# Kernel optimization log

Measured on AMD Instinct MI355X. Metric: run time of the kernel, lower is better.

Reference implementation:

```python
import jax, jax.numpy as jnp
import numpy as np

T = 4096
D = 512
H = 8
HD = D // H
DFF = D  # dim_ff = dmodel per module code
NUM_ACTIONS = 14
NUM_OBJECTS = 123
NEG = -1e9


def _layernorm(x, g, b, eps=1e-5):
    m = jnp.mean(x, axis=-1, keepdims=True)
    v = jnp.var(x, axis=-1, keepdims=True)
    return (x - m) / jnp.sqrt(v + eps) * g + b


def setup_inputs() -> dict:
    key = jax.random.key(0)
    ks = jax.random.split(key, 12)
    w = lambda k, s: (jax.random.normal(k, s) * 0.02).astype(jnp.float32)
    return {
        "action_seq": jax.random.randint(ks[0], (T, 2), 0, NUM_ACTIONS),
        "batch_id": jnp.sort(jax.random.randint(ks[1], (T,), 0, 16)),
        "W_type": w(ks[2], (NUM_ACTIONS, D)), "b_type": jnp.zeros((D,), jnp.float32),
        "W_arg": w(ks[3], (NUM_OBJECTS + 1, D)), "b_arg": jnp.zeros((D,), jnp.float32),
        "sos": jnp.zeros((D,), jnp.float32),
        "Wq": w(ks[4], (2, D, D)), "bq": jnp.zeros((2, D), jnp.float32),
        "Wk": w(ks[5], (2, D, D)), "bk": jnp.zeros((2, D), jnp.float32),
        "Wv": w(ks[6], (2, D, D)), "bv": jnp.zeros((2, D), jnp.float32),
        "Wo": w(ks[7], (2, D, D)), "bo": jnp.zeros((2, D), jnp.float32),
        "ln1_g": jnp.ones((2, D), jnp.float32), "ln1_b": jnp.zeros((2, D), jnp.float32),
        "W1": w(ks[8], (2, D, DFF)), "b1": jnp.zeros((2, DFF), jnp.float32),
        "W2": w(ks[9], (2, DFF, D)), "b2": jnp.zeros((2, D), jnp.float32),
        "ln2_g": jnp.ones((2, D), jnp.float32), "ln2_b": jnp.zeros((2, D), jnp.float32),
    }


def _forward(action_seq, batch_id, W_type, b_type, W_arg, b_arg, sos,
             Wq, bq, Wk, bk, Wv, bv, Wo, bo, ln1_g, ln1_b, W1, b1, W2, b2, ln2_g, ln2_b):
    Tn = action_seq.shape[0]
    dt = W_type.dtype
    # embeddings (one-hot @ W == Linear on one-hot)
    type_emb = jax.nn.one_hot(action_seq[:, 0], NUM_ACTIONS, dtype=dt) @ W_type + b_type
    arg_emb = jax.nn.one_hot(action_seq[:, 1] + 1, NUM_OBJECTS + 1, dtype=dt) @ W_arg + b_arg
    # position within each packed sequence (batch_id sorted-contiguous)
    seg_start = jnp.searchsorted(batch_id, batch_id, side='left')
    pos = (jnp.arange(Tn) - seg_start).astype(dt)
    div = jnp.exp(-jnp.log(10000.0) * jnp.arange(0, D, 2).astype(dt) / D)
    ang = pos[:, None] * div[None, :]
    pe = jnp.stack([jnp.sin(ang), jnp.cos(ang)], axis=-1).reshape(Tn, D)  # interleaved sin/cos
    x = jnp.concatenate([sos[None, :], type_emb + arg_emb + pe], axis=0)  # [T+1, D]
    T1 = Tn + 1
    # block-diagonal causal mask with prepended SOS token (always attendable)
    idx = jnp.arange(T1)
    bid1 = jnp.concatenate([jnp.full((1,), -1, dtype=batch_id.dtype), batch_id])
    allowed = (idx[:, None] >= idx[None, :]) & (bid1[:, None] == bid1[None, :])
    allowed = allowed | (idx[None, :] == 0)
    bias = jnp.where(allowed, 0.0, NEG).astype(dt)  # [T1, T1]
    scale = 1.0 / jnp.sqrt(jnp.asarray(HD, dtype=dt))
    for l in range(2):  # transformer_layer_a, transformer_layer_b
        q = (x @ Wq[l] + bq[l]).reshape(T1, H, HD)
        k = (x @ Wk[l] + bk[l]).reshape(T1, H, HD)
        v = (x @ Wv[l] + bv[l]).reshape(T1, H, HD)
        s = jnp.einsum('qhd,khd->hqk', q, k) * scale + bias[None, :, :]
        a = jax.nn.softmax(s, axis=-1)
        o = jnp.einsum('hqk,khd->qhd', a, v).reshape(T1, D) @ Wo[l] + bo[l]
        x = _layernorm(x + o, ln1_g[l], ln1_b[l])
        f = jax.nn.relu(x @ W1[l] + b1[l]) @ W2[l] + b2[l]
        x = _layernorm(x + f, ln2_g[l], ln2_b[l])
    return x  # [T+1, D]


def reference(action_seq, batch_id, W_type, b_type, W_arg, b_arg, sos,
              Wq, bq, Wk, bk, Wv, bv, Wo, bo, ln1_g, ln1_b, W1, b1, W2, b2, ln2_g, ln2_b):
    return _forward(action_seq, batch_id, W_type, b_type, W_arg, b_arg, sos,
                    Wq, bq, Wk, bk, Wv, bv, Wo, bo, ln1_g, ln1_b, W1, b1, W2, b2, ln2_g, ln2_b)
```

## Files before the change

kernel.cpp:

```cpp
#include <hip/hip_runtime.h>
#include <hip/hip_bf16.h>
#include <stdint.h>

#define T_TOK 4096
#define T1N   4097
#define DMODEL 512
#define VTS   4160

typedef __attribute__((ext_vector_type(8))) short bf16x8;
typedef __attribute__((ext_vector_type(4))) float f32x4;

static __device__ __forceinline__ unsigned short f2bf(float f) {
  __hip_bfloat16 h = __float2bfloat16(f);
  return *reinterpret_cast<unsigned short*>(&h);
}

__global__ __launch_bounds__(256) void wt_kernel(
    const float* __restrict__ Wq, const float* __restrict__ Wk,
    const float* __restrict__ Wv, const float* __restrict__ Wo,
    const float* __restrict__ W1, const float* __restrict__ W2,
    __hip_bfloat16* __restrict__ out) {
  int m = blockIdx.z;
  int kind = m >> 1, layer = m & 1;
  const float* src = kind==0?Wq: kind==1?Wk: kind==2?Wv: kind==3?Wo: kind==4?W1:W2;
  src += (size_t)layer*DMODEL*DMODEL;
  __hip_bfloat16* dst = out + (size_t)m*DMODEL*DMODEL;
  __shared__ float tile[32][33];
  int bn = blockIdx.x*32;
  int bk = blockIdx.y*32;
  int tx = threadIdx.x & 31, ty = threadIdx.x >> 5;
  for (int r = ty; r < 32; r += 8)
    tile[r][tx] = src[(size_t)(bk + r)*DMODEL + bn + tx];
  __syncthreads();
  for (int r = ty; r < 32; r += 8)
    dst[(size_t)(bn + r)*DMODEL + bk + tx] = __float2bfloat16(tile[tx][r]);
}

__global__ __launch_bounds__(256) void embed_kernel(
    const int* __restrict__ aseq, const int* __restrict__ bid,
    const float* __restrict__ Wt, const float* __restrict__ bt,
    const float* __restrict__ Wa, const float* __restrict__ ba,
    const float* __restrict__ sosv,
    float* __restrict__ x, __hip_bfloat16* __restrict__ xb,
    int* __restrict__ ss) {
  int i = blockIdx.x;
  int tid = threadIdx.x;
  int d0 = tid * 2;
  float o0, o1;
  if (i == 0) {
    o0 = sosv[d0]; o1 = sosv[d0+1];
  } else {
    int t = i - 1;
    int a0 = aseq[2*t], a1 = aseq[2*t+1];
    int key = bid[t];
    int lo = 0, hi = t;
    while (lo < hi) { int mid = (lo+hi) >> 1; if (bid[mid] < key) lo = mid + 1; else hi = mid; }
    if (tid == 0) ss[t] = lo;
    float pos = (float)(t - lo);
    float dv = __expf(-9.210340371976184f * (float)d0 * (1.0f/(float)DMODEL));
    float ang = pos * dv;
    float sn = sinf(ang), cs = cosf(ang);
    o0 = Wt[(size_t)a0*DMODEL + d0]   + bt[d0]   + Wa[(size_t)(a1+1)*DMODEL + d0]   + ba[d0]   + sn;
    o1 = Wt[(size_t)a0*DMODEL + d0+1] + bt[d0+1] + Wa[(size_t)(a1+1)*DMODEL + d0+1] + ba[d0+1] + cs;
  }
  size_t base = (size_t)i*DMODEL + d0;
  x[base] = o0; x[base+1] = o1;
  xb[base] = __float2bfloat16(o0); xb[base+1] = __float2bfloat16(o1);
}

template<int ACT, bool WF32, bool WB16>
__device__ __forceinline__ void gemm_body(
    const __hip_bfloat16* __restrict__ A, const __hip_bfloat16* __restrict__ Bt,
    const float* __restrict__ bias, float* __restrict__ Cf,
    __hip_bfloat16* __restrict__ Cb, int M) {
  constexpr int K = 512, N = 512;
  __shared__ __align__(16) __hip_bfloat16 As[64][72];
  __shared__ __align__(16) __hip_bfloat16 Bs[64][72];
  const int tid = threadIdx.x;
  const int m0 = blockIdx.x * 64;
  const int n0 = blockIdx.y * 64;
  const int lane = tid & 63, wave = tid >> 6;
  const int wm = wave >> 1, wn = wave & 1;
  f32x4 acc[2][2] = {};
  const int r0 = tid >> 3;
  const int koff = (tid & 7) * 8;
  const uint4 zero4 = {0,0,0,0};
  for (int k0 = 0; k0 < K; k0 += 64) {
    __syncthreads();
    #pragma unroll
    for (int rr = 0; rr < 2; rr++) {
      int row = r0 + rr*32;
      int grow = m0 + row;
      uint4 av = (grow < M) ? *(const uint4*)(A + (size_t)grow*K + k0 + koff) : zero4;
      *(uint4*)&As[row][koff] = av;
      uint4 bv = *(const uint4*)(Bt + (size_t)(n0+row)*K + k0 + koff);
      *(uint4*)&Bs[row][koff] = bv;
    }
    __syncthreads();
    #pragma unroll
    for (int kc = 0; kc < 64; kc += 32) {
      bf16x8 af[2], bf[2];
      #pragma unroll
      for (int i2 = 0; i2 < 2; i2++) {
        af[i2] = *(const bf16x8*)&As[wm*32 + i2*16 + (lane&15)][kc + (lane>>4)*8];
        bf[i2] = *(const bf16x8*)&Bs[wn*32 + i2*16 + (lane&15)][kc + (lane>>4)*8];
      }
      #pragma unroll
      for (int mi = 0; mi < 2; mi++)
        #pragma unroll
        for (int ni = 0; ni < 2; ni++)
          acc[mi][ni] = __builtin_amdgcn_mfma_f32_16x16x32_bf16(af[mi], bf[ni], acc[mi][ni], 0, 0, 0);
    }
  }
  #pragma unroll
  for (int mi = 0; mi < 2; mi++) {
    int rbase = m0 + wm*32 + mi*16 + ((lane>>4)<<2);
    #pragma unroll
    for (int ni = 0; ni < 2; ni++) {
      int col = n0 + wn*32 + ni*16 + (lane&15);
      float bb = bias[col];
      #pragma unroll
      for (int r = 0; r < 4; r++) {
        int row = rbase + r;
        if (row < M) {
          float val = acc[mi][ni][r] + bb;
          if (ACT == 1) val = fmaxf(val, 0.0f);
          if (WF32) Cf[(size_t)row*N + col] = val;
          if (WB16) Cb[(size_t)row*N + col] = __float2bfloat16(val);
        }
      }
    }
  }
}

template<int ACT, bool WF32, bool WB16>
__global__ __launch_bounds__(256) void gemm_one(
    const __hip_bfloat16* __restrict__ A, const __hip_bfloat16* __restrict__ Bt,
    const float* __restrict__ bias, float* __restrict__ Cf,
    __hip_bfloat16* __restrict__ Cb, int M) {
  gemm_body<ACT,WF32,WB16>(A, Bt, bias, Cf, Cb, M);
}

__global__ __launch_bounds__(256) void gemm_qkv(
    const __hip_bfloat16* __restrict__ A,
    const __hip_bfloat16* __restrict__ B0, const __hip_bfloat16* __restrict__ B1,
    const __hip_bfloat16* __restrict__ B2,
    const float* __restrict__ bias0, const float* __restrict__ bias1, const float* __restrict__ bias2,
    __hip_bfloat16* __restrict__ C0, __hip_bfloat16* __restrict__ C1, __hip_bfloat16* __restrict__ C2,
    int M) {
  int z = blockIdx.z;
  const __hip_bfloat16* Bt = (z==0) ? B0 : (z==1) ? B1 : B2;
  const float* bias = (z==0) ? bias0 : (z==1) ? bias1 : bias2;
  __hip_bfloat16* Cb = (z==0) ? C0 : (z==1) ? C1 : C2;
  gemm_body<0,false,true>(A, Bt, bias, nullptr, Cb, M);
}

__global__ __launch_bounds__(256) void vtrans_kernel(
    const short* __restrict__ vb, short* __restrict__ vt) {
  __shared__ short tile[64][72];
  int t0 = blockIdx.x*64, d0 = blockIdx.y*64;
  int c8 = threadIdx.x & 7, rr = threadIdx.x >> 3;
  #pragma unroll
  for (int i = 0; i < 2; i++) {
    int trow = rr + 32*i;
    bf16x8 val;
    if (t0 + trow < T1N) val = *(const bf16x8*)(vb + (size_t)(t0+trow)*DMODEL + d0 + c8*8);
    else val = (bf16x8){0,0,0,0,0,0,0,0};
    #pragma unroll
    for (int e = 0; e < 8; e++) tile[c8*8+e][trow] = val[e];
  }
  __syncthreads();
  #pragma unroll
  for (int i = 0; i < 2; i++) {
    int drow = rr + 32*i;
    bf16x8 oval = *(const bf16x8*)&tile[drow][c8*8];
    *(bf16x8*)(vt + (size_t)(d0+drow)*VTS + t0 + c8*8) = oval;
  }
}

__global__ __launch_bounds__(64) void attn_kernel(
    const __hip_bfloat16* __restrict__ q,
    const __hip_bfloat16* __restrict__ k,
    const __hip_bfloat16* __restrict__ vt,
    const int* __restrict__ ss,
    __hip_bfloat16* __restrict__ out) {
  const int h  = blockIdx.y;
  const int q0 = blockIdx.x * 16;
  const int lane = threadIdx.x;
  const int g  = lane >> 4;
  const int qi = lane & 15;
  const int qrow = q0 + qi;

  int qld = (qrow < T1N) ? qrow : (T1N-1);
  const __hip_bfloat16* qp = q + (size_t)qld*DMODEL + h*64 + g*8;
  bf16x8 qlo = *(const bf16x8*)qp;
  bf16x8 qhi = *(const bf16x8*)(qp + 32);

  int jl;
  if (qrow >= T1N)      jl = 0x7fffffff;
  else if (qrow == 0)   jl = 1;
  else                  jl = ss[qrow-1] + 1;

  const __hip_bfloat16* k0p = k + h*64 + g*8;
  float part = 0.0f;
  #pragma unroll
  for (int e = 0; e < 8; e++) {
    part += __bfloat162float(((const __hip_bfloat16*)&qlo)[e]) * __bfloat162float(k0p[e]);
    part += __bfloat162float(((const __hip_bfloat16*)&qhi)[e]) * __bfloat162float(k0p[e+32]);
  }
  part += __shfl_xor(part, 16);
  part += __shfl_xor(part, 32);
  float m = part * 0.125f;
  float lsum = 1.0f;
  f32x4 o[4];
  #pragma unroll
  for (int d = 0; d < 4; d++) {
    float v0 = __bfloat162float(vt[(size_t)(h*64 + d*16 + qi)*VTS]);
    o[d] = (f32x4){v0, v0, v0, v0};
  }

  const int mjl = (q0 == 0) ? 1 : (ss[q0-1] + 1);
  const int kb_lo = mjl & ~31;
  const int jmax = (q0 + 15 < T1N - 1) ? (q0 + 15) : (T1N - 1);

  const int src0 = ((g & 1) << 5) + qi;
  const bool hiHalf = (g >= 2);

  for (int kbb = kb_lo; kbb <= jmax; kbb += 32) {
    int kr0 = kbb + qi;       if (kr0 > T1N-1) kr0 = T1N-1;
    int kr1 = kbb + 16 + qi;  if (kr1 > T1N-1) kr1 = T1N-1;
    const __hip_bfloat16* kp0 = k + (size_t)kr0*DMODEL + h*64 + g*8;
    const __hip_bfloat16* kp1 = k + (size_t)kr1*DMODEL + h*64 + g*8;
    bf16x8 ka_lo = *(const bf16x8*)kp0, ka_hi = *(const bf16x8*)(kp0 + 32);
    bf16x8 kb_l  = *(const bf16x8*)kp1, kb_h  = *(const bf16x8*)(kp1 + 32);
    bf16x8 vf[4];
    #pragma unroll
    for (int d = 0; d < 4; d++)
      vf[d] = *(const bf16x8*)(vt + (size_t)(h*64 + d*16 + qi)*VTS + kbb + g*8);

    f32x4 sA = {0,0,0,0}, sB = {0,0,0,0};
    sA = __builtin_amdgcn_mfma_f32_16x16x32_bf16(ka_lo, qlo, sA, 0, 0, 0);
    sA = __builtin_amdgcn_mfma_f32_16x16x32_bf16(ka_hi, qhi, sA, 0, 0, 0);
    sB = __builtin_amdgcn_mfma_f32_16x16x32_bf16(kb_l,  qlo, sB, 0, 0, 0);
    sB = __builtin_amdgcn_mfma_f32_16x16x32_bf16(kb_h,  qhi, sB, 0, 0, 0);

    float s[8];
    const int kA = kbb + 4*g, kB = kA + 16;
    #pragma unroll
    for (int r = 0; r < 4; r++) {
      s[r]   = (kA + r >= jl && kA + r <= qrow) ? sA[r]*0.125f : -1e30f;
      s[4+r] = (kB + r >= jl && kB + r <= qrow) ? sB[r]*0.125f : -1e30f;
    }
    float mx = s[0];
    #pragma unroll
    for (int i = 1; i < 8; i++) mx = fmaxf(mx, s[i]);
    mx = fmaxf(mx, __shfl_xor(mx, 16));
    mx = fmaxf(mx, __shfl_xor(mx, 32));
    float mnew = fmaxf(m, mx);
    float corr = __expf(m - mnew);
    m = mnew;
    float p[8], psum = 0.0f;
    #pragma unroll
    for (int i = 0; i < 8; i++) { p[i] = __expf(s[i] - mnew); psum += p[i]; }
    psum += __shfl_xor(psum, 16);
    psum += __shfl_xor(psum, 32);
    lsum = lsum*corr + psum;

    bf16x8 pa;
    #pragma unroll
    for (int r = 0; r < 4; r++) {
      unsigned w = (unsigned)f2bf(p[r]) | ((unsigned)f2bf(p[4+r]) << 16);
      unsigned v0 = (unsigned)__shfl((int)w, src0);
      unsigned v1 = (unsigned)__shfl((int)w, src0 + 16);
      pa[r]     = (short)(hiHalf ? (v0 >> 16) : (v0 & 0xffff));
      pa[4 + r] = (short)(hiHalf ? (v1 >> 16) : (v1 & 0xffff));
    }

    float cq0 = __shfl(corr, 4*g + 0);
    float cq1 = __shfl(corr, 4*g + 1);
    float cq2 = __shfl(corr, 4*g + 2);
    float cq3 = __shfl(corr, 4*g + 3);
    f32x4 cqv = (f32x4){cq0, cq1, cq2, cq3};
    #pragma unroll
    for (int d = 0; d < 4; d++) o[d] *= cqv;

    #pragma unroll
    for (int d = 0; d < 4; d++)
      o[d] = __builtin_amdgcn_mfma_f32_16x16x32_bf16(pa, vf[d], o[d], 0, 0, 0);
  }

  float inv = 1.0f / lsum;
  float li0 = __shfl(inv, 4*g + 0);
  float li1 = __shfl(inv, 4*g + 1);
  float li2 = __shfl(inv, 4*g + 2);
  float li3 = __shfl(inv, 4*g + 3);
  f32x4 liv = (f32x4){li0, li1, li2, li3};
  #pragma unroll
  for (int r = 0; r < 4; r++) {
    int row = q0 + 4*g + r;
    if (row < T1N) {
      __hip_bfloat16* op = out + (size_t)row*DMODEL + h*64 + qi;
      #pragma unroll
      for (int d = 0; d < 4; d++) op[d*16] = __float2bfloat16(o[d][r] * liv[r]);
    }
  }
}

__global__ __launch_bounds__(256) void ln_kernel(
    const float* __restrict__ xin, const float* __restrict__ yin,
    const float* __restrict__ g, const float* __restrict__ b,
    float* __restrict__ xout, __hip_bfloat16* __restrict__ xbout) {
  int row = blockIdx.x;
  int tid = threadIdx.x;
  const float* xp = xin + (size_t)row*DMODEL;
  const float* yp = yin + (size_t)row*DMODEL;
  float v0 = xp[tid] + yp[tid];
  float v1 = xp[tid+256] + yp[tid+256];
  float s = v0 + v1, sq = v0*v0 + v1*v1;
  #pragma unroll
  for (int off = 1; off < 64; off <<= 1) {
    s  += __shfl_xor(s, off);
    sq += __shfl_xor(sq, off);
  }
  __shared__ float ls[4], lq[4];
  int wave = tid >> 6;
  if ((tid & 63) == 0) { ls[wave] = s; lq[wave] = sq; }
  __syncthreads();
  s  = ls[0] + ls[1] + ls[2] + ls[3];
  sq = lq[0] + lq[1] + lq[2] + lq[3];
  float mean = s * (1.0f/512.0f);
  float var  = sq * (1.0f/512.0f) - mean*mean;
  float rstd = rsqrtf(var + 1e-5f);
  float o0 = (v0 - mean)*rstd*g[tid]     + b[tid];
  float o1 = (v1 - mean)*rstd*g[tid+256] + b[tid+256];
  size_t base = (size_t)row*DMODEL;
  xout[base + tid]       = o0;
  xout[base + tid + 256] = o1;
  xbout[base + tid]       = __float2bfloat16(o0);
  xbout[base + tid + 256] = __float2bfloat16(o1);
}

extern "C" void kernel_launch(void* const* d_in, const int* in_sizes, int n_in,
                              void* d_out, int out_size, void* d_ws, size_t ws_size,
                              hipStream_t stream) {
  const int*   aseq   = (const int*)d_in[0];
  const int*   bid    = (const int*)d_in[1];
  const float* W_type = (const float*)d_in[2];
  const float* b_type = (const float*)d_in[3];
  const float* W_arg  = (const float*)d_in[4];
  const float* b_arg  = (const float*)d_in[5];
  const float* sosv   = (const float*)d_in[6];
  const float* Wq = (const float*)d_in[7];
  const float* bq = (const float*)d_in[8];
  const float* Wk = (const float*)d_in[9];
  const float* bk = (const float*)d_in[10];
  const float* Wv = (const float*)d_in[11];
  const float* bv = (const float*)d_in[12];
  const float* Wo = (const float*)d_in[13];
  const float* bo = (const float*)d_in[14];
  const float* ln1g = (const float*)d_in[15];
  const float* ln1b = (const float*)d_in[16];
  const float* W1 = (const float*)d_in[17];
  const float* b1 = (const float*)d_in[18];
  const float* W2 = (const float*)d_in[19];
  const float* b2 = (const float*)d_in[20];
  const float* ln2g = (const float*)d_in[21];
  const float* ln2b = (const float*)d_in[22];

  char* wsp = (char*)d_ws;
  size_t off = 0;
  auto alloc = [&](size_t bytes) -> void* {
    void* p = wsp + off; off += (bytes + 255) & ~(size_t)255; return p;
  };
  __hip_bfloat16* WT  = (__hip_bfloat16*)alloc((size_t)12*512*512*2);
  float* x            = (float*)alloc((size_t)T1N*DMODEL*4);
  __hip_bfloat16* xb  = (__hip_bfloat16*)alloc((size_t)T1N*DMODEL*2);
  __hip_bfloat16* qb  = (__hip_bfloat16*)alloc((size_t)T1N*DMODEL*2);
  __hip_bfloat16* kbf = (__hip_bfloat16*)alloc((size_t)T1N*DMODEL*2);
  __hip_bfloat16* vb  = (__hip_bfloat16*)alloc((size_t)T1N*DMODEL*2);
  __hip_bfloat16* vtb = (__hip_bfloat16*)alloc((size_t)512*VTS*2);
  float* y            = (float*)alloc((size_t)T1N*DMODEL*4);
  __hip_bfloat16* ab  = (__hip_bfloat16*)alloc((size_t)T1N*DMODEL*2);
  __hip_bfloat16* f1b = (__hip_bfloat16*)alloc((size_t)T1N*DMODEL*2);
  int* ss             = (int*)alloc((size_t)T_TOK*4);

  wt_kernel<<<dim3(16,16,12), 256, 0, stream>>>(Wq, Wk, Wv, Wo, W1, W2, WT);
  embed_kernel<<<dim3(T1N), 256, 0, stream>>>(aseq, bid, W_type, b_type, W_arg, b_arg, sosv, x, xb, ss);

  const size_t WSZ = (size_t)512*512;
  const dim3 ggrid(65, 8);
  for (int l = 0; l < 2; l++) {
    const __hip_bfloat16* Bq  = WT + (size_t)(0*2+l)*WSZ;
    const __hip_bfloat16* Bk  = WT + (size_t)(1*2+l)*WSZ;
    const __hip_bfloat16* Bv  = WT + (size_t)(2*2+l)*WSZ;
    const __hip_bfloat16* Bo  = WT + (size_t)(3*2+l)*WSZ;
    const __hip_bfloat16* Bf1 = WT + (size_t)(4*2+l)*WSZ;
    const __hip_bfloat16* Bf2 = WT + (size_t)(5*2+l)*WSZ;

    gemm_qkv<<<dim3(65,8,3), 256, 0, stream>>>(xb, Bq, Bk, Bv,
        bq + l*512, bk + l*512, bv + l*512, qb, kbf, vb, T1N);
    vtrans_kernel<<<dim3(65,8), 256, 0, stream>>>((const short*)vb, (short*)vtb);
    attn_kernel<<<dim3(257,8), 64, 0, stream>>>(qb, kbf, vtb, ss, ab);
    gemm_one<0,true,false><<<ggrid, 256, 0, stream>>>(ab, Bo, bo + l*512, y, nullptr, T1N);
    ln_kernel<<<dim3(T1N), 256, 0, stream>>>(x, y, ln1g + l*512, ln1b + l*512, x, xb);
    gemm_one<1,false,true><<<ggrid, 256, 0, stream>>>(xb, Bf1, b1 + l*512, nullptr, f1b, T1N);
    gemm_one<0,true,false><<<ggrid, 256, 0, stream>>>(f1b, Bf2, b2 + l*512, y, nullptr, T1N);
    float* xout = (l == 1) ? (float*)d_out : x;
    ln_kernel<<<dim3(T1N), 256, 0, stream>>>(x, y, ln2g + l*512, ln2b + l*512, xout, xb);
  }
}
```

Baseline: 217.8 us.

## Double-buffer GEMM LDS tiles and fuse V transpose into QKV GEMM

The shared GEMM body now keeps two LDS tile buffers. It prefetches the next K-slice into registers while MFMAs run on the current one, which cuts one barrier per iteration and hides global load latency. The V projection swaps its MFMA operands so that it writes V directly in the transposed layout that attention expects. This removes the separate transpose kernel and the intermediate V buffer. LDS use per block doubles, and the padded tail columns of the transposed V buffer are no longer zero-filled.

```diff
diff --git a/kernel.cpp b/kernel.cpp
--- a/kernel.cpp
+++ b/kernel.cpp
@@ -68,14 +68,15 @@
   xb[base] = __float2bfloat16(o0); xb[base+1] = __float2bfloat16(o1);
 }
 
-template<int ACT, bool WF32, bool WB16>
+typedef __hip_bfloat16 ldsbuf_t[2][64][72];
+
+template<int ACT, bool WF32, bool WB16, bool TO>
 __device__ __forceinline__ void gemm_body(
     const __hip_bfloat16* __restrict__ A, const __hip_bfloat16* __restrict__ Bt,
     const float* __restrict__ bias, float* __restrict__ Cf,
-    __hip_bfloat16* __restrict__ Cb, int M) {
+    __hip_bfloat16* __restrict__ Cb, int M,
+    ldsbuf_t& As, ldsbuf_t& Bs) {
   constexpr int K = 512, N = 512;
-  __shared__ __align__(16) __hip_bfloat16 As[64][72];
-  __shared__ __align__(16) __hip_bfloat16 Bs[64][72];
   const int tid = threadIdx.x;
   const int m0 = blockIdx.x * 64;
   const int n0 = blockIdx.y * 64;
@@ -85,16 +86,27 @@
   const int r0 = tid >> 3;
   const int koff = (tid & 7) * 8;
   const uint4 zero4 = {0,0,0,0};
-  for (int k0 = 0; k0 < K; k0 += 64) {
-    __syncthreads();
-    #pragma unroll
-    for (int rr = 0; rr < 2; rr++) {
-      int row = r0 + rr*32;
-      int grow = m0 + row;
-      uint4 av = (grow < M) ? *(const uint4*)(A + (size_t)grow*K + k0 + koff) : zero4;
-      *(uint4*)&As[row][koff] = av;
-      uint4 bv = *(const uint4*)(Bt + (size_t)(n0+row)*K + k0 + koff);
-      *(uint4*)&Bs[row][koff] = bv;
+  const int grow0 = m0 + r0, grow1 = m0 + r0 + 32;
+
+  uint4 avp[2], bvp[2];
+  avp[0] = (grow0 < M) ? *(const uint4*)(A + (size_t)grow0*K + koff) : zero4;
+  avp[1] = (grow1 < M) ? *(const uint4*)(A + (size_t)grow1*K + koff) : zero4;
+  bvp[0] = *(const uint4*)(Bt + (size_t)(n0+r0)*K + koff);
+  bvp[1] = *(const uint4*)(Bt + (size_t)(n0+r0+32)*K + koff);
+  *(uint4*)&As[0][r0][koff]    = avp[0];
+  *(uint4*)&As[0][r0+32][koff] = avp[1];
+  *(uint4*)&Bs[0][r0][koff]    = bvp[0];
+  *(uint4*)&Bs[0][r0+32][koff] = bvp[1];
+
+  int cur = 0;
+  #pragma unroll
+  for (int t = 0; t < 8; ++t) {
+    if (t < 7) {
+      const int k0n = (t+1)*64;
+      avp[0] = (grow0 < M) ? *(const uint4*)(A + (size_t)grow0*K + k0n + koff) : zero4;
+      avp[1] = (grow1 < M) ? *(const uint4*)(A + (size_t)grow1*K + k0n + koff) : zero4;
+      bvp[0] = *(const uint4*)(Bt + (size_t)(n0+r0)*K + k0n + koff);
+      bvp[1] = *(const uint4*)(Bt + (size_t)(n0+r0+32)*K + k0n + koff);
     }
     __syncthreads();
     #pragma unroll
@@ -102,31 +114,60 @@
       bf16x8 af[2], bf[2];
       #pragma unroll
       for (int i2 = 0; i2 < 2; i2++) {
-        af[i2] = *(const bf16x8*)&As[wm*32 + i2*16 + (lane&15)][kc + (lane>>4)*8];
-        bf[i2] = *(const bf16x8*)&Bs[wn*32 + i2*16 + (lane&15)][kc + (lane>>4)*8];
+        af[i2] = *(const bf16x8*)&As[cur][wm*32 + i2*16 + (lane&15)][kc + (lane>>4)*8];
+        bf[i2] = *(const bf16x8*)&Bs[cur][wn*32 + i2*16 + (lane&15)][kc + (lane>>4)*8];
       }
       #pragma unroll
-      for (int mi = 0; mi < 2; mi++)
+      for (int i = 0; i < 2; i++)
         #pragma unroll
-        for (int ni = 0; ni < 2; ni++)
-          acc[mi][ni] = __builtin_amdgcn_mfma_f32_16x16x32_bf16(af[mi], bf[ni], acc[mi][ni], 0, 0, 0);
-    }
-  }
-  #pragma unroll
-  for (int mi = 0; mi < 2; mi++) {
-    int rbase = m0 + wm*32 + mi*16 + ((lane>>4)<<2);
-    #pragma unroll
-    for (int ni = 0; ni < 2; ni++) {
-      int col = n0 + wn*32 + ni*16 + (lane&15);
-      float bb = bias[col];
+        for (int j = 0; j < 2; j++) {
+          if (TO) acc[i][j] = __builtin_amdgcn_mfma_f32_16x16x32_bf16(bf[i], af[j], acc[i][j], 0, 0, 0);
+          else    acc[i][j] = __builtin_amdgcn_mfma_f32_16x16x32_bf16(af[i], bf[j], acc[i][j], 0, 0, 0);
+        }
+    }
+    if (t < 7) {
+      *(uint4*)&As[cur^1][r0][koff]    = avp[0];
+      *(uint4*)&As[cur^1][r0+32][koff] = avp[1];
+      *(uint4*)&Bs[cur^1][r0][koff]    = bvp[0];
+      *(uint4*)&Bs[cur^1][r0+32][koff] = bvp[1];
+    }
+    cur ^= 1;
+  }
+
+  if (TO) {
+    #pragma unroll
+    for (int bi = 0; bi < 2; bi++) {
+      int rbase = n0 + wn*32 + bi*16 + ((lane>>4)<<2);
       #pragma unroll
-      for (int r = 0; r < 4; r++) {
-        int row = rbase + r;
-        if (row < M) {
-          float val = acc[mi][ni][r] + bb;
-          if (ACT == 1) val = fmaxf(val, 0.0f);
-          if (WF32) Cf[(size_t)row*N + col] = val;
-          if (WB16) Cb[(size_t)row*N + col] = __float2bfloat16(val);
+      for (int ai = 0; ai < 2; ai++) {
+        int colm = m0 + wm*32 + ai*16 + (lane&15);
+        if (colm < M) {
+          #pragma unroll
+          for (int r = 0; r < 4; r++) {
+            int rn = rbase + r;
+            float val = acc[bi][ai][r] + bias[rn];
+            Cb[(size_t)rn*VTS + colm] = __float2bfloat16(val);
+          }
+        }
+      }
+    }
+  } else {
+    #pragma unroll
+    for (int mi = 0; mi < 2; mi++) {
+      int rbase = m0 + wm*32 + mi*16 + ((lane>>4)<<2);
+      #pragma unroll
+      for (int ni = 0; ni < 2; ni++) {
+        int col = n0 + wn*32 + ni*16 + (lane&15);
+        float bb = bias[col];
+        #pragma unroll
+        for (int r = 0; r < 4; r++) {
+          int row = rbase + r;
+          if (row < M) {
+            float val = acc[mi][ni][r] + bb;
+            if (ACT == 1) val = fmaxf(val, 0.0f);
+            if (WF32) Cf[(size_t)row*N + col] = val;
+            if (WB16) Cb[(size_t)row*N + col] = __float2bfloat16(val);
+          }
         }
       }
     }
@@ -138,7 +179,9 @@
     const __hip_bfloat16* __restrict__ A, const __hip_bfloat16* __restrict__ Bt,
     const float* __restrict__ bias, float* __restrict__ Cf,
     __hip_bfloat16* __restrict__ Cb, int M) {
-  gemm_body<ACT,WF32,WB16>(A, Bt, bias, Cf, Cb, M);
+  __shared__ __align__(16) ldsbuf_t As;
+  __shared__ __align__(16) ldsbuf_t Bs;
+  gemm_body<ACT,WF32,WB16,false>(A, Bt, bias, Cf, Cb, M, As, Bs);
 }
 
 __global__ __launch_bounds__(256) void gemm_qkv(
@@ -146,35 +189,18 @@
     const __hip_bfloat16* __restrict__ B0, const __hip_bfloat16* __restrict__ B1,
     const __hip_bfloat16* __restrict__ B2,
     const float* __restrict__ bias0, const float* __restrict__ bias1, const float* __restrict__ bias2,
-    __hip_bfloat16* __restrict__ C0, __hip_bfloat16* __restrict__ C1, __hip_bfloat16* __restrict__ C2,
+    __hip_bfloat16* __restrict__ C0, __hip_bfloat16* __restrict__ C1, __hip_bfloat16* __restrict__ vt,
     int M) {
+  __shared__ __align__(16) ldsbuf_t As;
+  __shared__ __align__(16) ldsbuf_t Bs;
   int z = blockIdx.z;
-  const __hip_bfloat16* Bt = (z==0) ? B0 : (z==1) ? B1 : B2;
-  const float* bias = (z==0) ? bias0 : (z==1) ? bias1 : bias2;
-  __hip_bfloat16* Cb = (z==0) ? C0 : (z==1) ? C1 : C2;
-  gemm_body<0,false,true>(A, Bt, bias, nullptr, Cb, M);
-}
-
-__global__ __launch_bounds__(256) void vtrans_kernel(
-    const short* __restrict__ vb, short* __restrict__ vt) {
-  __shared__ short tile[64][72];
-  int t0 = blockIdx.x*64, d0 = blockIdx.y*64;
-  int c8 = threadIdx.x & 7, rr = threadIdx.x >> 3;
-  #pragma unroll
-  for (int i = 0; i < 2; i++) {
-    int trow = rr + 32*i;
-    bf16x8 val;
-    if (t0 + trow < T1N) val = *(const bf16x8*)(vb + (size_t)(t0+trow)*DMODEL + d0 + c8*8);
-    else val = (bf16x8){0,0,0,0,0,0,0,0};
-    #pragma unroll
-    for (int e = 0; e < 8; e++) tile[c8*8+e][trow] = val[e];
-  }
-  __syncthreads();
-  #pragma unroll
-  for (int i = 0; i < 2; i++) {
-    int drow = rr + 32*i;
-    bf16x8 oval = *(const bf16x8*)&tile[drow][c8*8];
-    *(bf16x8*)(vt + (size_t)(d0+drow)*VTS + t0 + c8*8) = oval;
+  if (z == 2) {
+    gemm_body<0,false,true,true>(A, B2, bias2, nullptr, vt, M, As, Bs);
+  } else {
+    const __hip_bfloat16* Bt = (z==0) ? B0 : B1;
+    const float* bias = (z==0) ? bias0 : bias1;
+    __hip_bfloat16* Cb = (z==0) ? C0 : C1;
+    gemm_body<0,false,true,false>(A, Bt, bias, nullptr, Cb, M, As, Bs);
   }
 }
 
@@ -377,7 +403,6 @@
   __hip_bfloat16* xb  = (__hip_bfloat16*)alloc((size_t)T1N*DMODEL*2);
   __hip_bfloat16* qb  = (__hip_bfloat16*)alloc((size_t)T1N*DMODEL*2);
   __hip_bfloat16* kbf = (__hip_bfloat16*)alloc((size_t)T1N*DMODEL*2);
-  __hip_bfloat16* vb  = (__hip_bfloat16*)alloc((size_t)T1N*DMODEL*2);
   __hip_bfloat16* vtb = (__hip_bfloat16*)alloc((size_t)512*VTS*2);
   float* y            = (float*)alloc((size_t)T1N*DMODEL*4);
   __hip_bfloat16* ab  = (__hip_bfloat16*)alloc((size_t)T1N*DMODEL*2);
@@ -398,8 +423,7 @@
     const __hip_bfloat16* Bf2 = WT + (size_t)(5*2+l)*WSZ;
 
     gemm_qkv<<<dim3(65,8,3), 256, 0, stream>>>(xb, Bq, Bk, Bv,
-        bq + l*512, bk + l*512, bv + l*512, qb, kbf, vb, T1N);
-    vtrans_kernel<<<dim3(65,8), 256, 0, stream>>>((const short*)vb, (short*)vtb);
+        bq + l*512, bk + l*512, bv + l*512, qb, kbf, vtb, T1N);
     attn_kernel<<<dim3(257,8), 64, 0, stream>>>(qb, kbf, vtb, ss, ab);
     gemm_one<0,true,false><<<ggrid, 256, 0, stream>>>(ab, Bo, bo + l*512, y, nullptr, T1N);
     ln_kernel<<<dim3(T1N), 256, 0, stream>>>(x, y, ln1g + l*512, ln1b + l*512, x, xb);
```

Measured after the change: 372.3 us. 1.71x slower.

## Fuse QKV GEMM with V transpose, merge prep kernels, prefetch attention K/V

Applied to the files above, without the earlier changes.

Merges the weight-transpose and embedding kernels into one launch. Rewrites the QKV GEMM so each block loads the A tile once and computes Q, K and V together. V is computed with the operands swapped so it can be written directly in transposed layout, which removes the separate vtrans kernel and the intermediate V buffer. The attention loop now software-prefetches the next K/V fragments into registers. The costs are higher register and LDS use in the fused GEMM, fewer blocks for it, and strided scalar stores for the transposed V output.

```diff
diff --git a/kernel.cpp b/kernel.cpp
--- a/kernel.cpp
+++ b/kernel.cpp
@@ -15,61 +15,63 @@
   return *reinterpret_cast<unsigned short*>(&h);
 }
 
-__global__ __launch_bounds__(256) void wt_kernel(
-    const float* __restrict__ Wq, const float* __restrict__ Wk,
-    const float* __restrict__ Wv, const float* __restrict__ Wo,
-    const float* __restrict__ W1, const float* __restrict__ W2,
-    __hip_bfloat16* __restrict__ out) {
-  int m = blockIdx.z;
-  int kind = m >> 1, layer = m & 1;
-  const float* src = kind==0?Wq: kind==1?Wk: kind==2?Wv: kind==3?Wo: kind==4?W1:W2;
-  src += (size_t)layer*DMODEL*DMODEL;
-  __hip_bfloat16* dst = out + (size_t)m*DMODEL*DMODEL;
-  __shared__ float tile[32][33];
-  int bn = blockIdx.x*32;
-  int bk = blockIdx.y*32;
-  int tx = threadIdx.x & 31, ty = threadIdx.x >> 5;
-  for (int r = ty; r < 32; r += 8)
-    tile[r][tx] = src[(size_t)(bk + r)*DMODEL + bn + tx];
-  __syncthreads();
-  for (int r = ty; r < 32; r += 8)
-    dst[(size_t)(bn + r)*DMODEL + bk + tx] = __float2bfloat16(tile[tx][r]);
-}
-
-__global__ __launch_bounds__(256) void embed_kernel(
+__global__ __launch_bounds__(256) void prep_kernel(
     const int* __restrict__ aseq, const int* __restrict__ bid,
     const float* __restrict__ Wt, const float* __restrict__ bt,
     const float* __restrict__ Wa, const float* __restrict__ ba,
     const float* __restrict__ sosv,
+    const float* __restrict__ Wq, const float* __restrict__ Wk,
+    const float* __restrict__ Wv, const float* __restrict__ Wo,
+    const float* __restrict__ W1, const float* __restrict__ W2,
     float* __restrict__ x, __hip_bfloat16* __restrict__ xb,
-    int* __restrict__ ss) {
-  int i = blockIdx.x;
-  int tid = threadIdx.x;
-  int d0 = tid * 2;
-  float o0, o1;
-  if (i == 0) {
-    o0 = sosv[d0]; o1 = sosv[d0+1];
+    int* __restrict__ ss, __hip_bfloat16* __restrict__ wtout) {
+  __shared__ float tile[32][33];
+  const int b = blockIdx.x;
+  const int tid = threadIdx.x;
+  if (b < T1N) {
+    int i = b;
+    int d0 = tid * 2;
+    float o0, o1;
+    if (i == 0) {
+      o0 = sosv[d0]; o1 = sosv[d0+1];
+    } else {
+      int t = i - 1;
+      int a0 = aseq[2*t], a1 = aseq[2*t+1];
+      int key = bid[t];
+      int lo = 0, hi = t;
+      while (lo < hi) { int mid = (lo+hi) >> 1; if (bid[mid] < key) lo = mid + 1; else hi = mid; }
+      if (tid == 0) ss[t] = lo;
+      float pos = (float)(t - lo);
+      float dv = __expf(-9.210340371976184f * (float)d0 * (1.0f/(float)DMODEL));
+      float ang = pos * dv;
+      float sn = sinf(ang), cs = cosf(ang);
+      o0 = Wt[(size_t)a0*DMODEL + d0]   + bt[d0]   + Wa[(size_t)(a1+1)*DMODEL + d0]   + ba[d0]   + sn;
+      o1 = Wt[(size_t)a0*DMODEL + d0+1] + bt[d0+1] + Wa[(size_t)(a1+1)*DMODEL + d0+1] + ba[d0+1] + cs;
+    }
+    size_t base = (size_t)i*DMODEL + d0;
+    x[base] = o0; x[base+1] = o1;
+    xb[base] = __float2bfloat16(o0); xb[base+1] = __float2bfloat16(o1);
   } else {
-    int t = i - 1;
-    int a0 = aseq[2*t], a1 = aseq[2*t+1];
-    int key = bid[t];
-    int lo = 0, hi = t;
-    while (lo < hi) { int mid = (lo+hi) >> 1; if (bid[mid] < key) lo = mid + 1; else hi = mid; }
-    if (tid == 0) ss[t] = lo;
-    float pos = (float)(t - lo);
-    float dv = __expf(-9.210340371976184f * (float)d0 * (1.0f/(float)DMODEL));
-    float ang = pos * dv;
-    float sn = sinf(ang), cs = cosf(ang);
-    o0 = Wt[(size_t)a0*DMODEL + d0]   + bt[d0]   + Wa[(size_t)(a1+1)*DMODEL + d0]   + ba[d0]   + sn;
-    o1 = Wt[(size_t)a0*DMODEL + d0+1] + bt[d0+1] + Wa[(size_t)(a1+1)*DMODEL + d0+1] + ba[d0+1] + cs;
-  }
-  size_t base = (size_t)i*DMODEL + d0;
-  x[base] = o0; x[base+1] = o1;
-  xb[base] = __float2bfloat16(o0); xb[base+1] = __float2bfloat16(o1);
+    int w = b - T1N;
+    int m = w >> 8;
+    int rem = w & 255;
+    int bn = (rem >> 4) * 32;
+    int bk = (rem & 15) * 32;
+    int kind = m >> 1, layer = m & 1;
+    const float* src = kind==0?Wq: kind==1?Wk: kind==2?Wv: kind==3?Wo: kind==4?W1:W2;
+    src += (size_t)layer*DMODEL*DMODEL;
+    __hip_bfloat16* dst = wtout + (size_t)m*DMODEL*DMODEL;
+    int tx = tid & 31, ty = tid >> 5;
+    for (int r = ty; r < 32; r += 8)
+      tile[r][tx] = src[(size_t)(bk + r)*DMODEL + bn + tx];
+    __syncthreads();
+    for (int r = ty; r < 32; r += 8)
+      dst[(size_t)(bn + r)*DMODEL + bk + tx] = __float2bfloat16(tile[tx][r]);
+  }
 }
 
 template<int ACT, bool WF32, bool WB16>
-__device__ __forceinline__ void gemm_body(
+__global__ __launch_bounds__(256) void gemm_one(
     const __hip_bfloat16* __restrict__ A, const __hip_bfloat16* __restrict__ Bt,
     const float* __restrict__ bias, float* __restrict__ Cf,
     __hip_bfloat16* __restrict__ Cb, int M) {
@@ -133,48 +135,100 @@
   }
 }
 
-template<int ACT, bool WF32, bool WB16>
-__global__ __launch_bounds__(256) void gemm_one(
-    const __hip_bfloat16* __restrict__ A, const __hip_bfloat16* __restrict__ Bt,
-    const float* __restrict__ bias, float* __restrict__ Cf,
-    __hip_bfloat16* __restrict__ Cb, int M) {
-  gemm_body<ACT,WF32,WB16>(A, Bt, bias, Cf, Cb, M);
-}
-
 __global__ __launch_bounds__(256) void gemm_qkv(
     const __hip_bfloat16* __restrict__ A,
     const __hip_bfloat16* __restrict__ B0, const __hip_bfloat16* __restrict__ B1,
     const __hip_bfloat16* __restrict__ B2,
     const float* __restrict__ bias0, const float* __restrict__ bias1, const float* __restrict__ bias2,
-    __hip_bfloat16* __restrict__ C0, __hip_bfloat16* __restrict__ C1, __hip_bfloat16* __restrict__ C2,
+    __hip_bfloat16* __restrict__ C0, __hip_bfloat16* __restrict__ C1, __hip_bfloat16* __restrict__ vt,
     int M) {
-  int z = blockIdx.z;
-  const __hip_bfloat16* Bt = (z==0) ? B0 : (z==1) ? B1 : B2;
-  const float* bias = (z==0) ? bias0 : (z==1) ? bias1 : bias2;
-  __hip_bfloat16* Cb = (z==0) ? C0 : (z==1) ? C1 : C2;
-  gemm_body<0,false,true>(A, Bt, bias, nullptr, Cb, M);
-}
-
-__global__ __launch_bounds__(256) void vtrans_kernel(
-    const short* __restrict__ vb, short* __restrict__ vt) {
-  __shared__ short tile[64][72];
-  int t0 = blockIdx.x*64, d0 = blockIdx.y*64;
-  int c8 = threadIdx.x & 7, rr = threadIdx.x >> 3;
-  #pragma unroll
-  for (int i = 0; i < 2; i++) {
-    int trow = rr + 32*i;
-    bf16x8 val;
-    if (t0 + trow < T1N) val = *(const bf16x8*)(vb + (size_t)(t0+trow)*DMODEL + d0 + c8*8);
-    else val = (bf16x8){0,0,0,0,0,0,0,0};
-    #pragma unroll
-    for (int e = 0; e < 8; e++) tile[c8*8+e][trow] = val[e];
-  }
-  __syncthreads();
-  #pragma unroll
-  for (int i = 0; i < 2; i++) {
-    int drow = rr + 32*i;
-    bf16x8 oval = *(const bf16x8*)&tile[drow][c8*8];
-    *(bf16x8*)(vt + (size_t)(d0+drow)*VTS + t0 + c8*8) = oval;
+  constexpr int K = 512;
+  __shared__ __align__(16) __hip_bfloat16 As[64][72];
+  __shared__ __align__(16) __hip_bfloat16 Bs[3][64][72];
+  const int tid = threadIdx.x;
+  const int m0 = blockIdx.x * 64;
+  const int n0 = blockIdx.y * 64;
+  const int lane = tid & 63, wave = tid >> 6;
+  const int wm = wave >> 1, wn = wave & 1;
+  f32x4 acc[3][2][2] = {};
+  const int r0 = tid >> 3;
+  const int koff = (tid & 7) * 8;
+  const uint4 zero4 = {0,0,0,0};
+  for (int k0 = 0; k0 < K; k0 += 64) {
+    __syncthreads();
+    #pragma unroll
+    for (int rr = 0; rr < 2; rr++) {
+      int row = r0 + rr*32;
+      int grow = m0 + row;
+      uint4 av = (grow < M) ? *(const uint4*)(A + (size_t)grow*K + k0 + koff) : zero4;
+      *(uint4*)&As[row][koff] = av;
+    }
+    #pragma unroll
+    for (int z = 0; z < 3; z++) {
+      const __hip_bfloat16* Bp = (z==0) ? B0 : (z==1) ? B1 : B2;
+      #pragma unroll
+      for (int rr = 0; rr < 2; rr++) {
+        int row = r0 + rr*32;
+        uint4 bv = *(const uint4*)(Bp + (size_t)(n0+row)*K + k0 + koff);
+        *(uint4*)&Bs[z][row][koff] = bv;
+      }
+    }
+    __syncthreads();
+    #pragma unroll
+    for (int kc = 0; kc < 64; kc += 32) {
+      bf16x8 af[2];
+      #pragma unroll
+      for (int i2 = 0; i2 < 2; i2++)
+        af[i2] = *(const bf16x8*)&As[wm*32 + i2*16 + (lane&15)][kc + (lane>>4)*8];
+      #pragma unroll
+      for (int z = 0; z < 3; z++) {
+        bf16x8 bf[2];
+        #pragma unroll
+        for (int i2 = 0; i2 < 2; i2++)
+          bf[i2] = *(const bf16x8*)&Bs[z][wn*32 + i2*16 + (lane&15)][kc + (lane>>4)*8];
+        #pragma unroll
+        for (int i = 0; i < 2; i++)
+          #pragma unroll
+          for (int j = 0; j < 2; j++) {
+            if (z == 2) acc[2][i][j] = __builtin_amdgcn_mfma_f32_16x16x32_bf16(bf[i], af[j], acc[2][i][j], 0, 0, 0);
+            else        acc[z][i][j] = __builtin_amdgcn_mfma_f32_16x16x32_bf16(af[i], bf[j], acc[z][i][j], 0, 0, 0);
+          }
+      }
+    }
+  }
+  #pragma unroll
+  for (int z = 0; z < 2; z++) {
+    __hip_bfloat16* Cz = (z==0) ? C0 : C1;
+    const float* bz = (z==0) ? bias0 : bias1;
+    #pragma unroll
+    for (int mi = 0; mi < 2; mi++) {
+      int rbase = m0 + wm*32 + mi*16 + ((lane>>4)<<2);
+      #pragma unroll
+      for (int ni = 0; ni < 2; ni++) {
+        int col = n0 + wn*32 + ni*16 + (lane&15);
+        float bb = bz[col];
+        #pragma unroll
+        for (int r = 0; r < 4; r++) {
+          int row = rbase + r;
+          if (row < M) Cz[(size_t)row*DMODEL + col] = __float2bfloat16(acc[z][mi][ni][r] + bb);
+        }
+      }
+    }
+  }
+  #pragma unroll
+  for (int bi = 0; bi < 2; bi++) {
+    int rbase = n0 + wn*32 + bi*16 + ((lane>>4)<<2);
+    #pragma unroll
+    for (int ai = 0; ai < 2; ai++) {
+      int colm = m0 + wm*32 + ai*16 + (lane&15);
+      if (colm < M) {
+        #pragma unroll
+        for (int r = 0; r < 4; r++) {
+          int rn = rbase + r;
+          vt[(size_t)rn*VTS + colm] = __float2bfloat16(acc[2][bi][ai][r] + bias2[rn]);
+        }
+      }
+    }
   }
 }
 
@@ -226,23 +280,43 @@
   const int src0 = ((g & 1) << 5) + qi;
   const bool hiHalf = (g >= 2);
 
-  for (int kbb = kb_lo; kbb <= jmax; kbb += 32) {
-    int kr0 = kbb + qi;       if (kr0 > T1N-1) kr0 = T1N-1;
-    int kr1 = kbb + 16 + qi;  if (kr1 > T1N-1) kr1 = T1N-1;
+  bf16x8 cka0, cka1, ckb0, ckb1, cv0, cv1, cv2, cv3;
+  {
+    int kr0 = kb_lo + qi;       if (kr0 > T1N-1) kr0 = T1N-1;
+    int kr1 = kb_lo + 16 + qi;  if (kr1 > T1N-1) kr1 = T1N-1;
     const __hip_bfloat16* kp0 = k + (size_t)kr0*DMODEL + h*64 + g*8;
     const __hip_bfloat16* kp1 = k + (size_t)kr1*DMODEL + h*64 + g*8;
-    bf16x8 ka_lo = *(const bf16x8*)kp0, ka_hi = *(const bf16x8*)(kp0 + 32);
-    bf16x8 kb_l  = *(const bf16x8*)kp1, kb_h  = *(const bf16x8*)(kp1 + 32);
-    bf16x8 vf[4];
-    #pragma unroll
-    for (int d = 0; d < 4; d++)
-      vf[d] = *(const bf16x8*)(vt + (size_t)(h*64 + d*16 + qi)*VTS + kbb + g*8);
+    cka0 = *(const bf16x8*)kp0; cka1 = *(const bf16x8*)(kp0 + 32);
+    ckb0 = *(const bf16x8*)kp1; ckb1 = *(const bf16x8*)(kp1 + 32);
+    const __hip_bfloat16* vp = vt + (size_t)(h*64 + qi)*VTS + kb_lo + g*8;
+    cv0 = *(const bf16x8*)vp;
+    cv1 = *(const bf16x8*)(vp + (size_t)16*VTS);
+    cv2 = *(const bf16x8*)(vp + (size_t)32*VTS);
+    cv3 = *(const bf16x8*)(vp + (size_t)48*VTS);
+  }
+
+  for (int kbb = kb_lo; kbb <= jmax; kbb += 32) {
+    int kn = (kbb + 32 <= jmax) ? (kbb + 32) : kbb;
+    bf16x8 nka0, nka1, nkb0, nkb1, nv0, nv1, nv2, nv3;
+    {
+      int kr0 = kn + qi;       if (kr0 > T1N-1) kr0 = T1N-1;
+      int kr1 = kn + 16 + qi;  if (kr1 > T1N-1) kr1 = T1N-1;
+      const __hip_bfloat16* kp0 = k + (size_t)kr0*DMODEL + h*64 + g*8;
+      const __hip_bfloat16* kp1 = k + (size_t)kr1*DMODEL + h*64 + g*8;
+      nka0 = *(const bf16x8*)kp0; nka1 = *(const bf16x8*)(kp0 + 32);
+      nkb0 = *(const bf16x8*)kp1; nkb1 = *(const bf16x8*)(kp1 + 32);
+      const __hip_bfloat16* vp = vt + (size_t)(h*64 + qi)*VTS + kn + g*8;
+      nv0 = *(const bf16x8*)vp;
+      nv1 = *(const bf16x8*)(vp + (size_t)16*VTS);
+      nv2 = *(const bf16x8*)(vp + (size_t)32*VTS);
+      nv3 = *(const bf16x8*)(vp + (size_t)48*VTS);
+    }
 
     f32x4 sA = {0,0,0,0}, sB = {0,0,0,0};
-    sA = __builtin_amdgcn_mfma_f32_16x16x32_bf16(ka_lo, qlo, sA, 0, 0, 0);
-    sA = __builtin_amdgcn_mfma_f32_16x16x32_bf16(ka_hi, qhi, sA, 0, 0, 0);
-    sB = __builtin_amdgcn_mfma_f32_16x16x32_bf16(kb_l,  qlo, sB, 0, 0, 0);
-    sB = __builtin_amdgcn_mfma_f32_16x16x32_bf16(kb_h,  qhi, sB, 0, 0, 0);
+    sA = __builtin_amdgcn_mfma_f32_16x16x32_bf16(cka0, qlo, sA, 0, 0, 0);
+    sA = __builtin_amdgcn_mfma_f32_16x16x32_bf16(cka1, qhi, sA, 0, 0, 0);
+    sB = __builtin_amdgcn_mfma_f32_16x16x32_bf16(ckb0, qlo, sB, 0, 0, 0);
+    sB = __builtin_amdgcn_mfma_f32_16x16x32_bf16(ckb1, qhi, sB, 0, 0, 0);
 
     float s[8];
     const int kA = kbb + 4*g, kB = kA + 16;
@@ -284,9 +358,13 @@
     #pragma unroll
     for (int d = 0; d < 4; d++) o[d] *= cqv;
 
-    #pragma unroll
-    for (int d = 0; d < 4; d++)
-      o[d] = __builtin_amdgcn_mfma_f32_16x16x32_bf16(pa, vf[d], o[d], 0, 0, 0);
+    o[0] = __builtin_amdgcn_mfma_f32_16x16x32_bf16(pa, cv0, o[0], 0, 0, 0);
+    o[1] = __builtin_amdgcn_mfma_f32_16x16x32_bf16(pa, cv1, o[1], 0, 0, 0);
+    o[2] = __builtin_amdgcn_mfma_f32_16x16x32_bf16(pa, cv2, o[2], 0, 0, 0);
+    o[3] = __builtin_amdgcn_mfma_f32_16x16x32_bf16(pa, cv3, o[3], 0, 0, 0);
+
+    cka0 = nka0; cka1 = nka1; ckb0 = nkb0; ckb1 = nkb1;
+    cv0 = nv0; cv1 = nv1; cv2 = nv2; cv3 = nv3;
   }
 
   float inv = 1.0f / lsum;
@@ -377,15 +455,15 @@
   __hip_bfloat16* xb  = (__hip_bfloat16*)alloc((size_t)T1N*DMODEL*2);
   __hip_bfloat16* qb  = (__hip_bfloat16*)alloc((size_t)T1N*DMODEL*2);
   __hip_bfloat16* kbf = (__hip_bfloat16*)alloc((size_t)T1N*DMODEL*2);
-  __hip_bfloat16* vb  = (__hip_bfloat16*)alloc((size_t)T1N*DMODEL*2);
   __hip_bfloat16* vtb = (__hip_bfloat16*)alloc((size_t)512*VTS*2);
   float* y            = (float*)alloc((size_t)T1N*DMODEL*4);
   __hip_bfloat16* ab  = (__hip_bfloat16*)alloc((size_t)T1N*DMODEL*2);
   __hip_bfloat16* f1b = (__hip_bfloat16*)alloc((size_t)T1N*DMODEL*2);
   int* ss             = (int*)alloc((size_t)T_TOK*4);
 
-  wt_kernel<<<dim3(16,16,12), 256, 0, stream>>>(Wq, Wk, Wv, Wo, W1, W2, WT);
-  embed_kernel<<<dim3(T1N), 256, 0, stream>>>(aseq, bid, W_type, b_type, W_arg, b_arg, sosv, x, xb, ss);
+  prep_kernel<<<dim3(T1N + 12*256), 256, 0, stream>>>(
+      aseq, bid, W_type, b_type, W_arg, b_arg, sosv,
+      Wq, Wk, Wv, Wo, W1, W2, x, xb, ss, WT);
 
   const size_t WSZ = (size_t)512*512;
   const dim3 ggrid(65, 8);
@@ -397,9 +475,8 @@
     const __hip_bfloat16* Bf1 = WT + (size_t)(4*2+l)*WSZ;
     const __hip_bfloat16* Bf2 = WT + (size_t)(5*2+l)*WSZ;
 
-    gemm_qkv<<<dim3(65,8,3), 256, 0, stream>>>(xb, Bq, Bk, Bv,
-        bq + l*512, bk + l*512, bv + l*512, qb, kbf, vb, T1N);
-    vtrans_kernel<<<dim3(65,8), 256, 0, stream>>>((const short*)vb, (short*)vtb);
+    gemm_qkv<<<ggrid, 256, 0, stream>>>(xb, Bq, Bk, Bv,
+        bq + l*512, bk + l*512, bv + l*512, qb, kbf, vtb, T1N);
     attn_kernel<<<dim3(257,8), 64, 0, stream>>>(qb, kbf, vtb, ss, ab);
     gemm_one<0,true,false><<<ggrid, 256, 0, stream>>>(ab, Bo, bo + l*512, y, nullptr, T1N);
     ln_kernel<<<dim3(T1N), 256, 0, stream>>>(x, y, ln1g + l*512, ln1b + l*512, x, xb);
```

Result: faster. 207.4 us (-4.8%).
